# Optimization experiments

Measured on AMD Instinct MI355X. Metric: run time of the kernel, lower is better.

The kernel has to match this reference:

```python
import jax, jax.numpy as jnp
import numpy as np

B, H, V = 4096, 2048, 32000
IGNORE_INDEX = -100
BETA = 0.1


def setup_inputs() -> dict:
    key = jax.random.key(0)
    kx, kw, ky = jax.random.split(key, 3)
    x = jax.random.normal(kx, (B, H), dtype=jnp.float32)
    # nn.Linear weight: shape (V, H), uniform(-1/sqrt(H), 1/sqrt(H))
    bound = 1.0 / np.sqrt(H)
    W = jax.random.uniform(kw, (V, H), dtype=jnp.float32, minval=-bound, maxval=bound)
    y = jax.random.randint(ky, (B,), 0, V, dtype=jnp.int64)
    return {"x": x, "W": W, "y": y}


def reference(x, W, y):
    # Linear projection: (B,H) @ (H,V) -> (B,V)
    logits = jnp.einsum("bh,vh->bv", x, W)
    half = logits.shape[0] // 2

    # Cross entropy (mean reduction, ignore_index) on the chosen half.
    logp = jax.nn.log_softmax(logits[:half], axis=-1)  # (half, V)
    y_half = y[:half]
    valid = y_half != IGNORE_INDEX
    safe_y = jnp.where(valid, y_half, 0)
    nll = -jnp.take_along_axis(logp, safe_y[:, None], axis=-1)[:, 0]
    nll = jnp.where(valid, nll, 0.0)
    ce_loss = nll.sum() / jnp.maximum(valid.sum(), 1).astype(nll.dtype)

    # Mean log-prob over the vocab dim for every row (as in the reference).
    all_logprobs = jax.nn.log_softmax(logits, axis=-1).mean(axis=-1)  # (B,)
    chosen = all_logprobs[:half]
    rejected = all_logprobs[half:]

    # ORPO odds-ratio loss
    log_odds = (chosen - rejected) - (
        jnp.log1p(-jnp.exp(chosen)) - jnp.log1p(-jnp.exp(rejected))
    )
    or_losses = BETA * jax.nn.log_sigmoid(log_odds)
    return ce_loss - or_losses.mean()
```

## Files before the change

kernel.cpp:

```cpp
#include <hip/hip_runtime.h>
#include <stdint.h>

#define BDIM 4096
#define HDIM 2048
#define VDIM 32000
#define HALF (BDIM / 2)
#define IGNORE_INDEX (-100)

typedef int   v8i  __attribute__((ext_vector_type(8)));
typedef int   v4i  __attribute__((ext_vector_type(4)));
typedef float v16f __attribute__((ext_vector_type(16)));
typedef float f32x4 __attribute__((ext_vector_type(4)));
typedef __bf16 bf16x8 __attribute__((ext_vector_type(8)));

#define AS1 __attribute__((address_space(1)))
#define AS3 __attribute__((address_space(3)))

__device__ __forceinline__ unsigned short f2bf(float f) {
    union { float f; unsigned int u; } v; v.f = f;
    unsigned int u = v.u;
    unsigned int r = u + 0x7FFFu + ((u >> 16) & 1u);
    return (unsigned short)(r >> 16);
}

__global__ void cvt_fp8_kernel(const float* __restrict__ x,
                               const float* __restrict__ W,
                               uint8_t* __restrict__ xq,
                               uint8_t* __restrict__ wq,
                               int nx4, int ntot4) {
    const int nth = gridDim.x * blockDim.x;
    const int t = blockIdx.x * blockDim.x + threadIdx.x;
    const int i0 = ((t >> 6) << 8) + (t & 63);
    const int stride = nth * 4;
    for (int i = i0; i < ntot4; i += stride) {
        const float4* s; unsigned* d; int j; float m;
        if (i < nx4) { s = (const float4*)x; d = (unsigned*)xq; j = i; m = 1.0f; }
        else         { s = (const float4*)W; d = (unsigned*)wq; j = i - nx4; m = 64.0f; }
        float4 f0 = s[j];
        float4 f1 = s[j + 64];
        float4 f2 = s[j + 128];
        float4 f3 = s[j + 192];
        int w;
        w = __builtin_amdgcn_cvt_pk_fp8_f32(f0.x * m, f0.y * m, 0, false);
        w = __builtin_amdgcn_cvt_pk_fp8_f32(f0.z * m, f0.w * m, w, true);
        d[j] = (unsigned)w;
        w = __builtin_amdgcn_cvt_pk_fp8_f32(f1.x * m, f1.y * m, 0, false);
        w = __builtin_amdgcn_cvt_pk_fp8_f32(f1.z * m, f1.w * m, w, true);
        d[j + 64] = (unsigned)w;
        w = __builtin_amdgcn_cvt_pk_fp8_f32(f2.x * m, f2.y * m, 0, false);
        w = __builtin_amdgcn_cvt_pk_fp8_f32(f2.z * m, f2.w * m, w, true);
        d[j + 128] = (unsigned)w;
        w = __builtin_amdgcn_cvt_pk_fp8_f32(f3.x * m, f3.y * m, 0, false);
        w = __builtin_amdgcn_cvt_pk_fp8_f32(f3.z * m, f3.w * m, w, true);
        d[j + 192] = (unsigned)w;
    }
}

__global__ __launch_bounds__(256, 4)
void gemm_reduce_fp8(const uint8_t* __restrict__ A, const uint8_t* __restrict__ B,
                     const int* __restrict__ y,
                     float* __restrict__ sumexp, float* __restrict__ sumlog,
                     float* __restrict__ tlog) {
    __shared__ uint8_t sA[2][128 * 64];
    __shared__ uint8_t sB[2][128 * 64];

    const int tid = threadIdx.x;
    const int lane = tid & 63;
    const int wave = tid >> 6;
    const int wm = wave >> 1, wn = wave & 1;
    const int m0 = blockIdx.x * 128;
    const int v0 = blockIdx.y * 128;

    v16f acc[2][2];
#pragma unroll
    for (int i = 0; i < 2; i++)
#pragma unroll
        for (int j = 0; j < 2; j++)
#pragma unroll
            for (int r = 0; r < 16; r++) acc[i][j][r] = 0.f;

    const int srow = wave * 32 + (lane >> 2);
    const int sc   = ((lane & 3) - ((lane >> 3) & 3)) & 3;
    const uint8_t* gA0 = A + (size_t)(m0 + srow) * HDIM + sc * 16;
    const uint8_t* gB0 = B + (size_t)(v0 + srow) * HDIM + sc * 16;
    const uint8_t* gA1 = gA0 + (size_t)16 * HDIM;
    const uint8_t* gB1 = gB0 + (size_t)16 * HDIM;
    const int lofs0 = (wave * 32) * 64;
    const int lofs1 = lofs0 + 16 * 64;

    const int fr32 = lane & 31;
    const int h = lane >> 5;
    const int swr = (fr32 >> 1) & 3;
    const int pos0 = (2 * h + swr) & 3;
    const int pos1 = (2 * h + 1 + swr) & 3;
    const int rA0 = (wm * 64 + fr32) * 64;
    const int rA1 = (wm * 64 + 32 + fr32) * 64;
    const int rB0 = (wn * 64 + fr32) * 64;
    const int rB1 = (wn * 64 + 32 + fr32) * 64;

    for (int kt = 0; kt < HDIM; kt += 128) {
        __builtin_amdgcn_global_load_lds((const AS1 unsigned int*)(gA0 + kt),
                                         (AS3 unsigned int*)&sA[0][lofs0], 16, 0, 0);
        __builtin_amdgcn_global_load_lds((const AS1 unsigned int*)(gA1 + kt),
                                         (AS3 unsigned int*)&sA[0][lofs1], 16, 0, 0);
        __builtin_amdgcn_global_load_lds((const AS1 unsigned int*)(gA0 + kt + 64),
                                         (AS3 unsigned int*)&sA[1][lofs0], 16, 0, 0);
        __builtin_amdgcn_global_load_lds((const AS1 unsigned int*)(gA1 + kt + 64),
                                         (AS3 unsigned int*)&sA[1][lofs1], 16, 0, 0);
        __builtin_amdgcn_global_load_lds((const AS1 unsigned int*)(gB0 + kt),
                                         (AS3 unsigned int*)&sB[0][lofs0], 16, 0, 0);
        __builtin_amdgcn_global_load_lds((const AS1 unsigned int*)(gB1 + kt),
                                         (AS3 unsigned int*)&sB[0][lofs1], 16, 0, 0);
        __builtin_amdgcn_global_load_lds((const AS1 unsigned int*)(gB0 + kt + 64),
                                         (AS3 unsigned int*)&sB[1][lofs0], 16, 0, 0);
        __builtin_amdgcn_global_load_lds((const AS1 unsigned int*)(gB1 + kt + 64),
                                         (AS3 unsigned int*)&sB[1][lofs1], 16, 0, 0);
        __syncthreads();

#pragma unroll
        for (int s = 0; s < 2; s++) {
            const v4i* pA0 = (const v4i*)&sA[s][rA0];
            const v4i* pA1 = (const v4i*)&sA[s][rA1];
            const v4i* pB0 = (const v4i*)&sB[s][rB0];
            const v4i* pB1 = (const v4i*)&sB[s][rB1];
            v4i a00 = pA0[pos0], a01 = pA0[pos1];
            v4i a10 = pA1[pos0], a11 = pA1[pos1];
            v4i b00 = pB0[pos0], b01 = pB0[pos1];
            v4i b10 = pB1[pos0], b11 = pB1[pos1];
            v8i af0 = {a00[0], a00[1], a00[2], a00[3], a01[0], a01[1], a01[2], a01[3]};
            v8i af1 = {a10[0], a10[1], a10[2], a10[3], a11[0], a11[1], a11[2], a11[3]};
            v8i bf0 = {b00[0], b00[1], b00[2], b00[3], b01[0], b01[1], b01[2], b01[3]};
            v8i bf1 = {b10[0], b10[1], b10[2], b10[3], b11[0], b11[1], b11[2], b11[3]};

            acc[0][0] = __builtin_amdgcn_mfma_scale_f32_32x32x64_f8f6f4(
                af0, bf0, acc[0][0], 0, 0, 0, 0x7F7F7F7F, 0, 0x7F7F7F7F);
            acc[0][1] = __builtin_amdgcn_mfma_scale_f32_32x32x64_f8f6f4(
                af0, bf1, acc[0][1], 0, 0, 0, 0x7F7F7F7F, 0, 0x7F7F7F7F);
            acc[1][0] = __builtin_amdgcn_mfma_scale_f32_32x32x64_f8f6f4(
                af1, bf0, acc[1][0], 0, 0, 0, 0x7F7F7F7F, 0, 0x7F7F7F7F);
            acc[1][1] = __builtin_amdgcn_mfma_scale_f32_32x32x64_f8f6f4(
                af1, bf1, acc[1][1], 0, 0, 0, 0x7F7F7F7F, 0, 0x7F7F7F7F);
        }
        __syncthreads();
    }

    const float s64 = 0.015625f;
#pragma unroll
    for (int mi = 0; mi < 2; mi++) {
        const int baseRow = m0 + wm * 64 + mi * 32;
#pragma unroll
        for (int reg = 0; reg < 16; reg++) {
            float va = acc[mi][0][reg] * s64;
            float vb = acc[mi][1][reg] * s64;
            float e = __expf(va) + __expf(vb);
            float sm = va + vb;
#pragma unroll
            for (int off = 1; off < 32; off <<= 1) {
                e  += __shfl_xor(e, off);
                sm += __shfl_xor(sm, off);
            }
            int row = baseRow + (reg & 3) + 8 * (reg >> 2) + 4 * h;
            if (fr32 == 0) {
                atomicAdd(&sumexp[row], e);
                atomicAdd(&sumlog[row], sm);
            }
            int yv = y[row];
            int c0 = v0 + wn * 64 + fr32;
            if (c0 == yv) tlog[row] = va;
            if (c0 + 32 == yv) tlog[row] = vb;
        }
    }
}

__global__ __launch_bounds__(256, 4)
void gemm_reduce_f32(const float* __restrict__ A, const float* __restrict__ B,
                     const int* __restrict__ y,
                     float* __restrict__ sumexp, float* __restrict__ sumlog,
                     float* __restrict__ tlog) {
    __shared__ unsigned short sA[128 * 32];
    __shared__ unsigned short sB[128 * 32];

    const int tid  = threadIdx.x;
    const int lane = tid & 63;
    const int wave = tid >> 6;
    const int wm = wave >> 1, wn = wave & 1;
    const int m0 = blockIdx.x * 128;
    const int v0 = blockIdx.y * 128;
    const int fr = lane & 15;
    const int fq = lane >> 4;
    const int swz = (fr >> 1) & 3;

    f32x4 acc[4][4];
#pragma unroll
    for (int i = 0; i < 4; i++)
#pragma unroll
        for (int j = 0; j < 4; j++) acc[i][j] = (f32x4){0.f, 0.f, 0.f, 0.f};

    const int r8 = tid >> 3;
    const int kc = (tid & 7) * 4;
    for (int kt = 0; kt < HDIM; kt += 32) {
#pragma unroll
        for (int p = 0; p < 4; p++) {
            int row = p * 32 + r8;
            int pos = ((kc >> 3) ^ ((row >> 1) & 3)) * 8 + (kc & 7);
            float4 fa = *(const float4*)&A[(size_t)(m0 + row) * HDIM + kt + kc];
            float4 fb = *(const float4*)&B[(size_t)(v0 + row) * HDIM + kt + kc];
            ushort4 ua, ub;
            ua.x = f2bf(fa.x); ua.y = f2bf(fa.y); ua.z = f2bf(fa.z); ua.w = f2bf(fa.w);
            ub.x = f2bf(fb.x); ub.y = f2bf(fb.y); ub.z = f2bf(fb.z); ub.w = f2bf(fb.w);
            *(ushort4*)&sA[row * 32 + pos] = ua;
            *(ushort4*)&sB[row * 32 + pos] = ub;
        }
        __syncthreads();

        bf16x8 af[4], bf[4];
#pragma unroll
        for (int i = 0; i < 4; i++) {
            af[i] = *(const bf16x8*)&sA[(wm * 64 + i * 16 + fr) * 32 + (fq ^ swz) * 8];
            bf[i] = *(const bf16x8*)&sB[(wn * 64 + i * 16 + fr) * 32 + (fq ^ swz) * 8];
        }
#pragma unroll
        for (int mi = 0; mi < 4; mi++)
#pragma unroll
            for (int ni = 0; ni < 4; ni++)
                acc[mi][ni] = __builtin_amdgcn_mfma_f32_16x16x32_bf16(
                    af[mi], bf[ni], acc[mi][ni], 0, 0, 0);
        __syncthreads();
    }

    const int baseRow = m0 + wm * 64;
    const int cbase = v0 + wn * 64 + fr;
#pragma unroll
    for (int mi = 0; mi < 4; mi++) {
        float se[4] = {0.f, 0.f, 0.f, 0.f};
        float sl[4] = {0.f, 0.f, 0.f, 0.f};
#pragma unroll
        for (int ni = 0; ni < 4; ni++)
#pragma unroll
            for (int r = 0; r < 4; r++) {
                float v = acc[mi][ni][r];
                se[r] += __expf(v);
                sl[r] += v;
            }
#pragma unroll
        for (int r = 0; r < 4; r++) {
            float e = se[r], s = sl[r];
#pragma unroll
            for (int off = 1; off < 16; off <<= 1) {
                e += __shfl_xor(e, off);
                s += __shfl_xor(s, off);
            }
            int row = baseRow + mi * 16 + fq * 4 + r;
            if (fr == 0) {
                atomicAdd(&sumexp[row], e);
                atomicAdd(&sumlog[row], s);
            }
            int yv = y[row];
#pragma unroll
            for (int ni = 0; ni < 4; ni++)
                if (cbase + ni * 16 == yv) tlog[row] = acc[mi][ni][r];
        }
    }
}

__global__ void finalize_kernel(const float* __restrict__ sumexp,
                                const float* __restrict__ sumlog,
                                const float* __restrict__ tlog,
                                const int* __restrict__ y,
                                float* __restrict__ out) {
    __shared__ float red[3][4];
    float s_nll = 0.f, s_or = 0.f, cnt = 0.f;
    for (int p = threadIdx.x; p < HALF; p += blockDim.x) {
        float lse_c = logf(sumexp[p]);
        float lse_r = logf(sumexp[p + HALF]);
        float mc = sumlog[p] * (1.0f / VDIM);
        float mr = sumlog[p + HALF] * (1.0f / VDIM);
        int yv = y[p];
        if (yv != IGNORE_INDEX) { s_nll += lse_c - tlog[p]; cnt += 1.f; }
        float ch = mc - lse_c, rj = mr - lse_r;
        float lo = (ch - rj) - (log1pf(-expf(ch)) - log1pf(-expf(rj)));
        float ls = fminf(lo, 0.f) - log1pf(expf(-fabsf(lo)));
        s_or += 0.1f * ls;
    }
    for (int off = 32; off; off >>= 1) {
        s_nll += __shfl_down(s_nll, off);
        s_or  += __shfl_down(s_or, off);
        cnt   += __shfl_down(cnt, off);
    }
    int wave = threadIdx.x >> 6, lane = threadIdx.x & 63;
    if (lane == 0) { red[0][wave] = s_nll; red[1][wave] = s_or; red[2][wave] = cnt; }
    __syncthreads();
    if (threadIdx.x == 0) {
        float tn = 0.f, to = 0.f, tc = 0.f;
        for (int w = 0; w < 4; w++) { tn += red[0][w]; to += red[1][w]; tc += red[2][w]; }
        out[0] = tn / fmaxf(tc, 1.f) - to / (float)HALF;
    }
}

extern "C" void kernel_launch(void* const* d_in, const int* in_sizes, int n_in,
                              void* d_out, int out_size, void* d_ws, size_t ws_size,
                              hipStream_t stream) {
    const float* x = (const float*)d_in[0];
    const float* W = (const float*)d_in[1];
    const int* y   = (const int*)d_in[2];
    float* out     = (float*)d_out;

    float* sumexp = (float*)d_ws;
    float* sumlog = sumexp + BDIM;
    float* tlog   = sumlog + BDIM;
    hipMemsetAsync(d_ws, 0, 3 * BDIM * sizeof(float), stream);

    const size_t bfoff = 65536;
    const size_t xcount = (size_t)BDIM * HDIM;
    const size_t wcount = (size_t)VDIM * HDIM;
    const size_t need = bfoff + xcount + wcount;

    dim3 grid(BDIM / 128, VDIM / 128);
    if (ws_size >= need) {
        uint8_t* xq = (uint8_t*)d_ws + bfoff;
        uint8_t* wq = xq + xcount;
        int nx4 = (int)(xcount / 4);
        int ntot4 = (int)((xcount + wcount) / 4);
        cvt_fp8_kernel<<<4096, 256, 0, stream>>>(x, W, xq, wq, nx4, ntot4);
        gemm_reduce_fp8<<<grid, 256, 0, stream>>>(xq, wq, y, sumexp, sumlog, tlog);
    } else {
        gemm_reduce_f32<<<grid, 256, 0, stream>>>(x, W, y, sumexp, sumlog, tlog);
    }
    finalize_kernel<<<1, 256, 0, stream>>>(sumexp, sumlog, tlog, y, out);
}
```

Baseline: 812.0 us.

## Double-buffer FP8 GEMM K-loop with async LDS prefetch and setprio

Restructures the K loop of the FP8 MFMA GEMM into a software pipeline. Each 64-wide K chunk is loaded into one of two LDS buffers while the other is consumed, gated by explicit vmcnt waits and raw s_barrier instead of __syncthreads after every load batch. MFMA issue is wrapped in s_setprio to favor matrix work. This aims to hide global-to-LDS latency, at the cost of relying on hand-counted vmcnt values and manual barriers, which are fragile.

Result: slower. 868.9 us (+7.0%).

```diff
diff --git a/kernel.cpp b/kernel.cpp
--- a/kernel.cpp
+++ b/kernel.cpp
@@ -98,51 +98,63 @@
     const int rB0 = (wn * 64 + fr32) * 64;
     const int rB1 = (wn * 64 + 32 + fr32) * 64;
 
-    for (int kt = 0; kt < HDIM; kt += 128) {
-        __builtin_amdgcn_global_load_lds((const AS1 unsigned int*)(gA0 + kt),
-                                         (AS3 unsigned int*)&sA[0][lofs0], 16, 0, 0);
-        __builtin_amdgcn_global_load_lds((const AS1 unsigned int*)(gA1 + kt),
-                                         (AS3 unsigned int*)&sA[0][lofs1], 16, 0, 0);
-        __builtin_amdgcn_global_load_lds((const AS1 unsigned int*)(gA0 + kt + 64),
-                                         (AS3 unsigned int*)&sA[1][lofs0], 16, 0, 0);
-        __builtin_amdgcn_global_load_lds((const AS1 unsigned int*)(gA1 + kt + 64),
-                                         (AS3 unsigned int*)&sA[1][lofs1], 16, 0, 0);
-        __builtin_amdgcn_global_load_lds((const AS1 unsigned int*)(gB0 + kt),
-                                         (AS3 unsigned int*)&sB[0][lofs0], 16, 0, 0);
-        __builtin_amdgcn_global_load_lds((const AS1 unsigned int*)(gB1 + kt),
-                                         (AS3 unsigned int*)&sB[0][lofs1], 16, 0, 0);
-        __builtin_amdgcn_global_load_lds((const AS1 unsigned int*)(gB0 + kt + 64),
-                                         (AS3 unsigned int*)&sB[1][lofs0], 16, 0, 0);
-        __builtin_amdgcn_global_load_lds((const AS1 unsigned int*)(gB1 + kt + 64),
-                                         (AS3 unsigned int*)&sB[1][lofs1], 16, 0, 0);
-        __syncthreads();
-
-#pragma unroll
-        for (int s = 0; s < 2; s++) {
-            const v4i* pA0 = (const v4i*)&sA[s][rA0];
-            const v4i* pA1 = (const v4i*)&sA[s][rA1];
-            const v4i* pB0 = (const v4i*)&sB[s][rB0];
-            const v4i* pB1 = (const v4i*)&sB[s][rB1];
-            v4i a00 = pA0[pos0], a01 = pA0[pos1];
-            v4i a10 = pA1[pos0], a11 = pA1[pos1];
-            v4i b00 = pB0[pos0], b01 = pB0[pos1];
-            v4i b10 = pB1[pos0], b11 = pB1[pos1];
-            v8i af0 = {a00[0], a00[1], a00[2], a00[3], a01[0], a01[1], a01[2], a01[3]};
-            v8i af1 = {a10[0], a10[1], a10[2], a10[3], a11[0], a11[1], a11[2], a11[3]};
-            v8i bf0 = {b00[0], b00[1], b00[2], b00[3], b01[0], b01[1], b01[2], b01[3]};
-            v8i bf1 = {b10[0], b10[1], b10[2], b10[3], b11[0], b11[1], b11[2], b11[3]};
-
-            acc[0][0] = __builtin_amdgcn_mfma_scale_f32_32x32x64_f8f6f4(
-                af0, bf0, acc[0][0], 0, 0, 0, 0x7F7F7F7F, 0, 0x7F7F7F7F);
-            acc[0][1] = __builtin_amdgcn_mfma_scale_f32_32x32x64_f8f6f4(
-                af0, bf1, acc[0][1], 0, 0, 0, 0x7F7F7F7F, 0, 0x7F7F7F7F);
-            acc[1][0] = __builtin_amdgcn_mfma_scale_f32_32x32x64_f8f6f4(
-                af1, bf0, acc[1][0], 0, 0, 0, 0x7F7F7F7F, 0, 0x7F7F7F7F);
-            acc[1][1] = __builtin_amdgcn_mfma_scale_f32_32x32x64_f8f6f4(
-                af1, bf1, acc[1][1], 0, 0, 0, 0x7F7F7F7F, 0, 0x7F7F7F7F);
-        }
-        __syncthreads();
-    }
+#define STAGE(BUF, KT) do {                                                     \
+        __builtin_amdgcn_global_load_lds(                                       \
+            (const AS1 unsigned int*)(gA0 + (size_t)(KT) * 64),                 \
+            (AS3 unsigned int*)(&sA[BUF][lofs0]), 16, 0, 0);                    \
+        __builtin_amdgcn_global_load_lds(                                       \
+            (const AS1 unsigned int*)(gA1 + (size_t)(KT) * 64),                 \
+            (AS3 unsigned int*)(&sA[BUF][lofs1]), 16, 0, 0);                    \
+        __builtin_amdgcn_global_load_lds(                                       \
+            (const AS1 unsigned int*)(gB0 + (size_t)(KT) * 64),                 \
+            (AS3 unsigned int*)(&sB[BUF][lofs0]), 16, 0, 0);                    \
+        __builtin_amdgcn_global_load_lds(                                       \
+            (const AS1 unsigned int*)(gB1 + (size_t)(KT) * 64),                 \
+            (AS3 unsigned int*)(&sB[BUF][lofs1]), 16, 0, 0);                    \
+    } while (0)
+
+#define KSTEP(BUF, VMASM) do {                                                  \
+        asm volatile(VMASM ::: "memory");                                       \
+        __builtin_amdgcn_sched_barrier(0);                                      \
+        __builtin_amdgcn_s_barrier();                                           \
+        const v4i* pA0 = (const v4i*)&sA[BUF][rA0];                             \
+        const v4i* pA1 = (const v4i*)&sA[BUF][rA1];                             \
+        const v4i* pB0 = (const v4i*)&sB[BUF][rB0];                             \
+        const v4i* pB1 = (const v4i*)&sB[BUF][rB1];                             \
+        v4i a00 = pA0[pos0], a01 = pA0[pos1];                                   \
+        v4i a10 = pA1[pos0], a11 = pA1[pos1];                                   \
+        v4i b00 = pB0[pos0], b01 = pB0[pos1];                                   \
+        v4i b10 = pB1[pos0], b11 = pB1[pos1];                                   \
+        v8i af0 = {a00[0], a00[1], a00[2], a00[3], a01[0], a01[1], a01[2], a01[3]}; \
+        v8i af1 = {a10[0], a10[1], a10[2], a10[3], a11[0], a11[1], a11[2], a11[3]}; \
+        v8i bf0 = {b00[0], b00[1], b00[2], b00[3], b01[0], b01[1], b01[2], b01[3]}; \
+        v8i bf1 = {b10[0], b10[1], b10[2], b10[3], b11[0], b11[1], b11[2], b11[3]}; \
+        __builtin_amdgcn_s_setprio(1);                                          \
+        acc[0][0] = __builtin_amdgcn_mfma_scale_f32_32x32x64_f8f6f4(            \
+            af0, bf0, acc[0][0], 0, 0, 0, 0x7F7F7F7F, 0, 0x7F7F7F7F);           \
+        acc[0][1] = __builtin_amdgcn_mfma_scale_f32_32x32x64_f8f6f4(            \
+            af0, bf1, acc[0][1], 0, 0, 0, 0x7F7F7F7F, 0, 0x7F7F7F7F);           \
+        acc[1][0] = __builtin_amdgcn_mfma_scale_f32_32x32x64_f8f6f4(            \
+            af1, bf0, acc[1][0], 0, 0, 0, 0x7F7F7F7F, 0, 0x7F7F7F7F);           \
+        acc[1][1] = __builtin_amdgcn_mfma_scale_f32_32x32x64_f8f6f4(            \
+            af1, bf1, acc[1][1], 0, 0, 0, 0x7F7F7F7F, 0, 0x7F7F7F7F);           \
+        __builtin_amdgcn_s_setprio(0);                                          \
+        __builtin_amdgcn_s_barrier();                                           \
+    } while (0)
+
+    STAGE(0, 0);
+    for (int kt = 0; kt < 30; kt += 2) {
+        STAGE(1, kt + 1);
+        KSTEP(0, "s_waitcnt vmcnt(4)");
+        STAGE(0, kt + 2);
+        KSTEP(1, "s_waitcnt vmcnt(4)");
+    }
+    STAGE(1, 31);
+    KSTEP(0, "s_waitcnt vmcnt(4)");
+    KSTEP(1, "s_waitcnt vmcnt(0)");
+
+#undef STAGE
+#undef KSTEP
 
     const float s64 = 0.015625f;
 #pragma unroll
```
